# Kernel tuning notes

Measured on AMD Instinct MI355X. Metric: run time of the kernel, lower is better.

Reference implementation:

```python
import jax, jax.numpy as jnp
import numpy as np

B, S, D = 1, 2048, 2048
E, K, F = 16, 4, 512
EPS = 1e-6


def setup_inputs() -> dict:
    key = jax.random.key(0)
    ks = jax.random.split(key, 5)
    return {
        "hidden_states": jax.random.normal(ks[0], (B, S, D), dtype=jnp.float32),
        "norm_weight": jnp.ones((D,), dtype=jnp.float32),
        "gate_w": jax.random.normal(ks[1], (E, D), dtype=jnp.float32) * 0.02,
        "w_gate": jax.random.normal(ks[2], (E, D, F), dtype=jnp.float32) * 0.02,
        "w_up": jax.random.normal(ks[3], (E, D, F), dtype=jnp.float32) * 0.02,
        "w_down": jax.random.normal(ks[4], (E, F, D), dtype=jnp.float32) * 0.02,
    }


def _rmsnorm(x, w, eps=EPS):
    xf = x.astype(jnp.float32)
    var = jnp.mean(xf * xf, axis=-1, keepdims=True)
    return (xf * jax.lax.rsqrt(var + eps)).astype(x.dtype) * w


def reference(hidden_states, norm_weight, gate_w, w_gate, w_up, w_down):
    residual = hidden_states
    h = _rmsnorm(hidden_states, norm_weight)
    x = h.reshape(-1, D)                                  # [T, D], T = B*S
    T = x.shape[0]

    # Router: softmax over experts (fp32), top-k, renormalize top-k weights.
    logits = x @ gate_w.T                                  # [T, E]
    probs = jax.nn.softmax(logits.astype(jnp.float32), axis=-1)
    top_w, top_i = jax.lax.top_k(probs, K)                 # [T, K]
    top_w = top_w / jnp.sum(top_w, axis=-1, keepdims=True)
    top_w = top_w.astype(x.dtype)

    # Dense combine matrix [T, E]: routing weight if selected, else 0.
    comb = jnp.zeros((T, E), dtype=x.dtype)
    comb = comb.at[jnp.arange(T)[:, None], top_i].add(top_w)

    # Experts: SiLU-gated MLP per expert, combined with routing weights.
    g = jnp.einsum("td,edf->tef", x, w_gate)               # [T, E, F]
    u = jnp.einsum("td,edf->tef", x, w_up)                 # [T, E, F]
    act = jax.nn.silu(g) * u                               # [T, E, F]
    # Weight per-expert contributions then project down.
    y = jnp.einsum("tef,efd,te->td", act, w_down, comb)    # [T, D]

    out = residual + y.reshape(B, S, D)
    return out
```

## Files before the change

### kernel.cpp

```cpp
#include <hip/hip_runtime.h>
#include <cstdint>
#include <cstddef>

#define T_ 2048
#define D_ 2048
#define E_ 16
#define F_ 512

typedef unsigned short u16;
typedef unsigned int u32;
typedef unsigned long long u64;
typedef __attribute__((ext_vector_type(8))) short bf16x8;
typedef __attribute__((ext_vector_type(4))) float f32x4;
typedef __attribute__((ext_vector_type(2))) u32 u32x2;
typedef __attribute__((ext_vector_type(4))) u32 u32x4;
typedef __attribute__((ext_vector_type(8))) u16 u16x8;
typedef __attribute__((ext_vector_type(4))) u16 u16x4;

__device__ __forceinline__ u16 f2bf(float f){
  union { float f; u32 u; } c; c.f = f;
  return (u16)((c.u + 0x7FFFu + ((c.u >> 16) & 1u)) >> 16);
}

__device__ __forceinline__ void gload16(const void* g, void* l){
  __builtin_amdgcn_global_load_lds((const __attribute__((address_space(1))) void*)g,
                                   (__attribute__((address_space(3))) void*)l,
                                   16, 0, 0);
}

__device__ __forceinline__ u32 pk2(float a, float b){
  u32 r;
  asm("v_cvt_pk_bf16_f32 %0, %1, %2" : "=v"(r) : "v"(a), "v"(b));
  return r;
}

__global__ __launch_bounds__(256) void k_transpose_all(
    const float* __restrict__ wg, const float* __restrict__ wu, const float* __restrict__ wd,
    u16* __restrict__ wgT, u16* __restrict__ wuT, u16* __restrict__ wdT)
{
  const int bid = blockIdx.x;
  const int mat = bid >> 11;
  const int rem = bid & 2047;
  const int e = rem >> 7, within = rem & 127;
  int R, C, r0, c0;
  const float* src;
  u16* dst;
  if (mat < 2){
    R = D_; C = F_;
    r0 = (within >> 3) * 128;  c0 = (within & 7) * 64;
    src = (mat == 0) ? wg : wu;
    dst = (mat == 0) ? wgT : wuT;
  } else {
    R = F_; C = D_;
    r0 = (within & 3) * 128;  c0 = (within >> 2) * 64;
    src = wd; dst = wdT;
  }
  const int tid = threadIdx.x;
  const int br = tid >> 4;
  const int bc = tid & 15;

  const float* s = src + ((size_t)e*R + r0 + br*8)*C + c0 + bc*4;
  float col[4][8];
  #pragma unroll
  for (int j = 0; j < 8; ++j){
    const float4 t = *(const float4*)(s + (size_t)j*C);
    col[0][j] = t.x; col[1][j] = t.y; col[2][j] = t.z; col[3][j] = t.w;
  }
  u16* d = dst + ((size_t)e*C + c0 + bc*4)*R + r0 + br*8;
  #pragma unroll
  for (int c = 0; c < 4; ++c){
    u32x4 o = { pk2(col[c][0], col[c][1]), pk2(col[c][2], col[c][3]),
                pk2(col[c][4], col[c][5]), pk2(col[c][6], col[c][7]) };
    *(u32x4*)(d + (size_t)c*R) = o;
  }
}

__global__ __launch_bounds__(256) void k_norm_router(
    const float* __restrict__ x, const float* __restrict__ nw, const float* __restrict__ gw,
    u16* __restrict__ h, int* __restrict__ tok_e, float* __restrict__ tok_w)
{
  const int t = blockIdx.x, tid = threadIdx.x;
  const int lane = tid & 63, wid = tid >> 6;
  const int d0 = tid * 8;
  const float4 v0 = *(const float4*)(x + (size_t)t*D_ + d0);
  const float4 v1 = *(const float4*)(x + (size_t)t*D_ + d0 + 4);
  float hv[8] = {v0.x, v0.y, v0.z, v0.w, v1.x, v1.y, v1.z, v1.w};
  float ss = 0.f;
  #pragma unroll
  for (int j = 0; j < 8; ++j) ss += hv[j]*hv[j];
  #pragma unroll
  for (int o = 32; o; o >>= 1) ss += __shfl_xor(ss, o);
  __shared__ float sred[4];
  __shared__ float red16[4][16];
  __shared__ float lf[16];
  if (lane == 0) sred[wid] = ss;
  __syncthreads();
  const float rstd = rsqrtf((sred[0]+sred[1]+sred[2]+sred[3]) * (1.f/(float)D_) + 1e-6f);
  const float4 w0 = *(const float4*)(nw + d0);
  const float4 w1 = *(const float4*)(nw + d0 + 4);
  const float wv[8] = {w0.x,w0.y,w0.z,w0.w,w1.x,w1.y,w1.z,w1.w};
  #pragma unroll
  for (int j = 0; j < 8; ++j) hv[j] = hv[j] * rstd * wv[j];
  u16x8 hb;
  #pragma unroll
  for (int j = 0; j < 8; ++j) hb[j] = f2bf(hv[j]);
  *(u16x8*)(h + (size_t)t*D_ + d0) = hb;

  float lg[16];
  #pragma unroll
  for (int e = 0; e < 16; ++e){
    const float4 g0 = *(const float4*)(gw + e*D_ + d0);
    const float4 g1 = *(const float4*)(gw + e*D_ + d0 + 4);
    lg[e] = hv[0]*g0.x + hv[1]*g0.y + hv[2]*g0.z + hv[3]*g0.w
          + hv[4]*g1.x + hv[5]*g1.y + hv[6]*g1.z + hv[7]*g1.w;
  }
  #pragma unroll
  for (int e = 0; e < 16; ++e){
    #pragma unroll
    for (int o = 32; o; o >>= 1) lg[e] += __shfl_xor(lg[e], o);
  }
  if (lane == 0){
    #pragma unroll
    for (int e = 0; e < 16; ++e) red16[wid][e] = lg[e];
  }
  __syncthreads();
  if (tid < 16) lf[tid] = red16[0][tid] + red16[1][tid] + red16[2][tid] + red16[3][tid];
  __syncthreads();
  if (tid == 0){
    float l[16];
    #pragma unroll
    for (int e = 0; e < 16; ++e) l[e] = lf[e];
    int sel[4]; float sv[4]; u32 used = 0;
    for (int k = 0; k < 4; ++k){
      float b = -3.4e38f; int bi = 0;
      for (int e = 0; e < 16; ++e)
        if (!((used >> e) & 1u) && l[e] > b){ b = l[e]; bi = e; }
      used |= 1u << bi; sel[k] = bi; sv[k] = b;
    }
    float ex[4]; float s = 0.f;
    for (int k = 0; k < 4; ++k){ ex[k] = __expf(sv[k] - sv[0]); s += ex[k]; }
    const float inv = 1.f / s;
    int4 te = {sel[0], sel[1], sel[2], sel[3]};
    float4 tw4 = {ex[0]*inv, ex[1]*inv, ex[2]*inv, ex[3]*inv};
    *(int4*)(tok_e + t*4) = te;
    *(float4*)(tok_w + t*4) = tw4;
  }
}

__global__ __launch_bounds__(256) void k_build_lists(
    const int* __restrict__ tok_e, const float* __restrict__ tok_w,
    int* __restrict__ eidx, float* __restrict__ ew, int* __restrict__ counts)
{
  const int e = blockIdx.x, tid = threadIdx.x;
  const int lane = tid & 63, wid = tid >> 6;
  __shared__ int wtot[4];
  __shared__ int base;
  if (tid == 0) base = 0;
  __syncthreads();
  for (int t0 = 0; t0 < T_; t0 += 256){
    const int t = t0 + tid;
    const int4 te = *(const int4*)(tok_e + t*4);
    const float4 tw = *(const float4*)(tok_w + t*4);
    bool m = false; float wv = 0.f;
    if      (te.x == e){ m = true; wv = tw.x; }
    else if (te.y == e){ m = true; wv = tw.y; }
    else if (te.z == e){ m = true; wv = tw.z; }
    else if (te.w == e){ m = true; wv = tw.w; }
    const u64 mask = __ballot(m);
    const int pre = __popcll(mask & ((1ull << lane) - 1ull));
    if (lane == 0) wtot[wid] = __popcll(mask);
    __syncthreads();
    int wbase = base;
    for (int i = 0; i < wid; ++i) wbase += wtot[i];
    if (m){
      eidx[e*T_ + wbase + pre] = t;
      ew[e*T_ + wbase + pre] = wv;
    }
    __syncthreads();
    if (tid == 0) base += wtot[0] + wtot[1] + wtot[2] + wtot[3];
    __syncthreads();
  }
  if (tid == 0) counts[e] = base;
}

__global__ __launch_bounds__(256) void k_slots(
    const int* __restrict__ counts, const int* __restrict__ eidx,
    const int* __restrict__ tok_e, int* __restrict__ tok_slot)
{
  const int e = blockIdx.x;
  int abase = 0;
  for (int i = 0; i < e; ++i) abase += counts[i];
  const int cnt = counts[e];
  for (int s = threadIdx.x; s < cnt; s += 256){
    const int t = eidx[e*T_ + s];
    const int4 te = *(const int4*)(tok_e + t*4);
    const int kidx = (te.x == e) ? 0 : (te.y == e) ? 1 : (te.z == e) ? 2 : 3;
    tok_slot[t*4 + kidx] = abase + s;
  }
}

__global__ __launch_bounds__(128, 2) void k_gateup(
    const u16* __restrict__ h, const u16* __restrict__ wgT, const u16* __restrict__ wuT,
    const int* __restrict__ counts, const int* __restrict__ eidx, const float* __restrict__ ew,
    u16* __restrict__ act)
{
  const int bid = blockIdx.x;
  const int tt = bid >> 7;
  const int e  = (bid >> 3) & 15;
  const int ft = bid & 7;

  const int cnt = counts[e];
  const int row0 = tt * 128;
  if (row0 >= cnt) return;
  int abase = 0;
  for (int i = 0; i < e; ++i) abase += counts[i];

  const int tid = threadIdx.x, lane = tid & 63, w = tid >> 6;
  const int f0 = ft * 64;

  __shared__ __align__(16) u16 Xs[3][4096];
  __shared__ __align__(16) u16 Ws[3][4096];

  int* toksS = (int*)&Xs[0][0];
  if (tid < 128){
    const int slot = row0 + tid;
    const int cs = slot < cnt ? slot : (cnt - 1);
    toksS[tid] = eidx[e*T_ + cs];
  }
  __syncthreads();

  const int lr = lane >> 2, lc = lane & 3;
  const int csw = lc ^ (lr & 3) ^ ((lr >> 2) & 3);

  const u16* srcX[4]; const u16* srcW[4]; u32 dof[4];
  #pragma unroll
  for (int q = 0; q < 4; ++q){
    const int r = w*64 + q*16 + lr;
    srcX[q] = h + (size_t)toksS[r]*D_ + 8*csw;
    const u16* wb = (r < 64) ? (wgT + ((size_t)e*F_ + f0 + r)*D_)
                             : (wuT + ((size_t)e*F_ + f0 + (r - 64))*D_);
    srcW[q] = wb + 8*csw;
    dof[q] = (u32)((w*64 + q*16) * 32);
  }
  __syncthreads();

  const int p = lane & 15, g4 = lane >> 4;
  u32 aB[4], bB[8];
  #pragma unroll
  for (int m = 0; m < 4; ++m) aB[m] = (u32)((w*64 + m*16 + p) * 32);
  #pragma unroll
  for (int n = 0; n < 8; ++n) bB[n] = (u32)((n*16 + p) * 32);
  const u32 s8 = 8u * (u32)(g4 ^ (p & 3) ^ ((p >> 2) & 3));

  f32x4 acc[4][8] = {};

  #pragma unroll
  for (int b = 0; b < 2; ++b){
    const int kb = b * 32;
    #pragma unroll
    for (int q = 0; q < 4; ++q){
      gload16(srcX[q] + kb, (void*)&Xs[b][dof[q]]);
      gload16(srcW[q] + kb, (void*)&Ws[b][dof[q]]);
    }
  }

  const int NSTEP = D_ / 32;
  int cur = 0;
  for (int kt = 0; kt < NSTEP; ++kt){
    if (kt < NSTEP - 1) asm volatile("s_waitcnt vmcnt(8)" ::: "memory");
    else                asm volatile("s_waitcnt vmcnt(0)" ::: "memory");
    __builtin_amdgcn_sched_barrier(0);
    __builtin_amdgcn_s_barrier();
    __builtin_amdgcn_sched_barrier(0);
    if (kt + 2 < NSTEP){
      const int kb2 = (kt + 2) * 32;
      int nb = cur + 2; if (nb >= 3) nb -= 3;
      #pragma unroll
      for (int q = 0; q < 4; ++q){
        gload16(srcX[q] + kb2, (void*)&Xs[nb][dof[q]]);
        gload16(srcW[q] + kb2, (void*)&Ws[nb][dof[q]]);
      }
    }
    const u16* Xp = &Xs[cur][0];
    const u16* Wp = &Ws[cur][0];
    bf16x8 aF[4], bF[8];
    #pragma unroll
    for (int m = 0; m < 4; ++m) aF[m] = *(const bf16x8*)&Xp[aB[m] + s8];
    #pragma unroll
    for (int n = 0; n < 8; ++n) bF[n] = *(const bf16x8*)&Wp[bB[n] + s8];
    #pragma unroll
    for (int m = 0; m < 4; ++m)
      #pragma unroll
      for (int n = 0; n < 8; ++n)
        acc[m][n] = __builtin_amdgcn_mfma_f32_16x16x32_bf16(aF[m], bF[n], acc[m][n], 0, 0, 0);
    cur = (cur == 2) ? 0 : cur + 1;
  }

  #pragma unroll
  for (int m = 0; m < 4; ++m)
    #pragma unroll
    for (int r = 0; r < 4; ++r){
      const int row  = w*64 + m*16 + g4*4 + r;
      const int slot = row0 + row;
      if (slot < cnt){
        const float tw = ew[e*T_ + slot];
        #pragma unroll
        for (int n = 0; n < 4; ++n){
          const float gv = acc[m][n][r], uv = acc[m][n+4][r];
          const float a = tw * (gv / (1.f + __expf(-gv))) * uv;
          act[(size_t)(abase + slot)*F_ + f0 + n*16 + p] = f2bf(a);
        }
      }
    }
}

__global__ __launch_bounds__(128, 2) void k_down(
    const u16* __restrict__ act, const u16* __restrict__ wdT,
    const int* __restrict__ counts, u16* __restrict__ ydown)
{
  const int bid = blockIdx.x;
  const int tt = bid >> 8;
  const int e  = (bid >> 4) & 15;
  const int dt = bid & 15;

  const int cnt = counts[e], row0 = tt * 128;
  if (row0 >= cnt) return;
  int abase = 0;
  for (int i = 0; i < e; ++i) abase += counts[i];

  const int tid = threadIdx.x, lane = tid & 63, w = tid >> 6;
  const int d0 = dt * 128;

  __shared__ __align__(16) u16 As[3][4096];
  __shared__ __align__(16) u16 Wd[3][4096];

  const int lr = lane >> 2, lc = lane & 3;
  const int csw = lc ^ (lr & 3) ^ ((lr >> 2) & 3);

  const u16* srcX[4]; const u16* srcW[4]; u32 dof[4];
  #pragma unroll
  for (int q = 0; q < 4; ++q){
    const int r = w*64 + q*16 + lr;
    const int rs = (row0 + r < cnt) ? (row0 + r) : (cnt - 1);
    srcX[q] = act + (size_t)(abase + rs)*F_ + 8*csw;
    srcW[q] = wdT + ((size_t)e*D_ + d0 + r)*F_ + 8*csw;
    dof[q] = (u32)((w*64 + q*16) * 32);
  }

  const int p = lane & 15, g4 = lane >> 4;
  u32 aB[4], bB[8];
  #pragma unroll
  for (int m = 0; m < 4; ++m) aB[m] = (u32)((w*64 + m*16 + p) * 32);
  #pragma unroll
  for (int n = 0; n < 8; ++n) bB[n] = (u32)((n*16 + p) * 32);
  const u32 s8 = 8u * (u32)(g4 ^ (p & 3) ^ ((p >> 2) & 3));

  f32x4 acc[4][8] = {};

  #pragma unroll
  for (int b = 0; b < 2; ++b){
    const int kb = b * 32;
    #pragma unroll
    for (int q = 0; q < 4; ++q){
      gload16(srcX[q] + kb, (void*)&As[b][dof[q]]);
      gload16(srcW[q] + kb, (void*)&Wd[b][dof[q]]);
    }
  }

  const int NSTEP = F_ / 32;
  int cur = 0;
  for (int kt = 0; kt < NSTEP; ++kt){
    if (kt < NSTEP - 1) asm volatile("s_waitcnt vmcnt(8)" ::: "memory");
    else                asm volatile("s_waitcnt vmcnt(0)" ::: "memory");
    __builtin_amdgcn_sched_barrier(0);
    __builtin_amdgcn_s_barrier();
    __builtin_amdgcn_sched_barrier(0);
    if (kt + 2 < NSTEP){
      const int kb2 = (kt + 2) * 32;
      int nb = cur + 2; if (nb >= 3) nb -= 3;
      #pragma unroll
      for (int q = 0; q < 4; ++q){
        gload16(srcX[q] + kb2, (void*)&As[nb][dof[q]]);
        gload16(srcW[q] + kb2, (void*)&Wd[nb][dof[q]]);
      }
    }
    const u16* Ap = &As[cur][0];
    const u16* Wp = &Wd[cur][0];
    bf16x8 aF[4], bF[8];
    #pragma unroll
    for (int m = 0; m < 4; ++m) aF[m] = *(const bf16x8*)&Ap[aB[m] + s8];
    #pragma unroll
    for (int n = 0; n < 8; ++n) bF[n] = *(const bf16x8*)&Wp[bB[n] + s8];
    #pragma unroll
    for (int m = 0; m < 4; ++m)
      #pragma unroll
      for (int n = 0; n < 8; ++n)
        acc[m][n] = __builtin_amdgcn_mfma_f32_16x16x32_bf16(aF[m], bF[n], acc[m][n], 0, 0, 0);
    cur = (cur == 2) ? 0 : cur + 1;
  }

  #pragma unroll
  for (int m = 0; m < 4; ++m){
    #pragma unroll
    for (int r = 0; r < 4; ++r){
      const int row  = w*64 + m*16 + g4*4 + r;
      const int slot = row0 + row;
      if (slot < cnt){
        u16* yp = ydown + (size_t)(abase + slot)*D_ + d0;
        #pragma unroll
        for (int n = 0; n < 8; ++n)
          yp[n*16 + p] = f2bf(acc[m][n][r]);
      }
    }
  }
}

__global__ __launch_bounds__(256) void k_combine(
    const float* __restrict__ x, const u16* __restrict__ ydown,
    const int* __restrict__ tok_slot, float* __restrict__ out)
{
  const int t = blockIdx.x;
  const int d0 = threadIdx.x * 8;
  const int4 sl = *(const int4*)(tok_slot + t*4);
  const float4 x0 = *(const float4*)(x + (size_t)t*D_ + d0);
  const float4 x1 = *(const float4*)(x + (size_t)t*D_ + d0 + 4);
  float s[8] = {x0.x, x0.y, x0.z, x0.w, x1.x, x1.y, x1.z, x1.w};
  const int sls[4] = {sl.x, sl.y, sl.z, sl.w};
  #pragma unroll
  for (int k = 0; k < 4; ++k){
    const u16x8 v = *(const u16x8*)(ydown + (size_t)sls[k]*D_ + d0);
    #pragma unroll
    for (int j = 0; j < 8; ++j){
      union { u32 u; float f; } c; c.u = (u32)v[j] << 16;
      s[j] += c.f;
    }
  }
  float4 o0 = {s[0], s[1], s[2], s[3]};
  float4 o1 = {s[4], s[5], s[6], s[7]};
  *(float4*)(out + (size_t)t*D_ + d0)     = o0;
  *(float4*)(out + (size_t)t*D_ + d0 + 4) = o1;
}

extern "C" void kernel_launch(void* const* d_in, const int* in_sizes, int n_in,
                              void* d_out, int out_size, void* d_ws, size_t ws_size,
                              hipStream_t stream)
{
  (void)in_sizes; (void)n_in; (void)out_size; (void)ws_size;
  const float* x     = (const float*)d_in[0];
  const float* nw    = (const float*)d_in[1];
  const float* gw    = (const float*)d_in[2];
  const float* wgate = (const float*)d_in[3];
  const float* wup   = (const float*)d_in[4];
  const float* wdown = (const float*)d_in[5];
  float* out = (float*)d_out;

  char* ws = (char*)d_ws;
  u16*   h        = (u16*)(ws);
  u16*   act      = (u16*)(ws + 8388608);
  int*   counts   = (int*)(ws + 16908288);
  int*   eidx     = (int*)(ws + 16908352);
  float* ew       = (float*)(ws + 17039424);
  int*   tok_e    = (int*)(ws + 17170496);
  float* tok_w    = (float*)(ws + 17203264);
  int*   tok_slot = (int*)(ws + 17236032);
  u16*   wgT      = (u16*)(ws + 17268800);
  u16*   wuT      = (u16*)(ws + 50823232);
  u16*   wdT      = (u16*)(ws + 84377664);
  u16*   ydown    = (u16*)(ws + 17268800);

  k_transpose_all<<<6144, 256, 0, stream>>>(wgate, wup, wdown, wgT, wuT, wdT);
  k_norm_router<<<T_, 256, 0, stream>>>(x, nw, gw, h, tok_e, tok_w);
  k_build_lists<<<E_, 256, 0, stream>>>(tok_e, tok_w, eidx, ew, counts);
  k_slots<<<E_, 256, 0, stream>>>(counts, eidx, tok_e, tok_slot);
  k_gateup<<<2048, 128, 0, stream>>>(h, wgT, wuT, counts, eidx, ew, act);
  k_down<<<4096, 128, 0, stream>>>(act, wdT, counts, ydown);
  k_combine<<<T_, 256, 0, stream>>>(x, ydown, tok_slot, out);
}
```

Measured before the change: 209.2 us.

## Fuse fp32 weight transpose and bf16 conversion into the expert GEMM loaders

Removes the separate pre-pass that transposed and converted all expert weights to bf16. The gate/up and down GEMM kernels now read fp32 weights straight from global memory into registers, convert them to bf16, and write them into swizzled LDS with a double-buffered register-staged pipeline. This saves a full read-write pass over all weights. In exchange, each GEMM block re-reads fp32 weights at twice the bytes, once per token tile, and the weight prefetch is now synchronous through registers.

```diff
diff --git a/kernel.cpp b/kernel.cpp
--- a/kernel.cpp
+++ b/kernel.cpp
@@ -15,7 +15,6 @@
 typedef __attribute__((ext_vector_type(2))) u32 u32x2;
 typedef __attribute__((ext_vector_type(4))) u32 u32x4;
 typedef __attribute__((ext_vector_type(8))) u16 u16x8;
-typedef __attribute__((ext_vector_type(4))) u16 u16x4;
 
 __device__ __forceinline__ u16 f2bf(float f){
   union { float f; u32 u; } c; c.f = f;
@@ -32,47 +31,6 @@
   u32 r;
   asm("v_cvt_pk_bf16_f32 %0, %1, %2" : "=v"(r) : "v"(a), "v"(b));
   return r;
-}
-
-__global__ __launch_bounds__(256) void k_transpose_all(
-    const float* __restrict__ wg, const float* __restrict__ wu, const float* __restrict__ wd,
-    u16* __restrict__ wgT, u16* __restrict__ wuT, u16* __restrict__ wdT)
-{
-  const int bid = blockIdx.x;
-  const int mat = bid >> 11;
-  const int rem = bid & 2047;
-  const int e = rem >> 7, within = rem & 127;
-  int R, C, r0, c0;
-  const float* src;
-  u16* dst;
-  if (mat < 2){
-    R = D_; C = F_;
-    r0 = (within >> 3) * 128;  c0 = (within & 7) * 64;
-    src = (mat == 0) ? wg : wu;
-    dst = (mat == 0) ? wgT : wuT;
-  } else {
-    R = F_; C = D_;
-    r0 = (within & 3) * 128;  c0 = (within >> 2) * 64;
-    src = wd; dst = wdT;
-  }
-  const int tid = threadIdx.x;
-  const int br = tid >> 4;
-  const int bc = tid & 15;
-
-  const float* s = src + ((size_t)e*R + r0 + br*8)*C + c0 + bc*4;
-  float col[4][8];
-  #pragma unroll
-  for (int j = 0; j < 8; ++j){
-    const float4 t = *(const float4*)(s + (size_t)j*C);
-    col[0][j] = t.x; col[1][j] = t.y; col[2][j] = t.z; col[3][j] = t.w;
-  }
-  u16* d = dst + ((size_t)e*C + c0 + bc*4)*R + r0 + br*8;
-  #pragma unroll
-  for (int c = 0; c < 4; ++c){
-    u32x4 o = { pk2(col[c][0], col[c][1]), pk2(col[c][2], col[c][3]),
-                pk2(col[c][4], col[c][5]), pk2(col[c][6], col[c][7]) };
-    *(u32x4*)(d + (size_t)c*R) = o;
-  }
 }
 
 __global__ __launch_bounds__(256) void k_norm_router(
@@ -199,8 +157,27 @@
   }
 }
 
+#define WLOAD(KB, SRC, S) do {                                                 \
+    _Pragma("unroll")                                                          \
+    for (int j = 0; j < 8; ++j){                                               \
+      const float4 t_ = *(const float4*)((SRC) + (size_t)((KB) + ko*8 + j)*(S));\
+      wvf[0][j]=t_.x; wvf[1][j]=t_.y; wvf[2][j]=t_.z; wvf[3][j]=t_.w;          \
+    }                                                                          \
+  } while (0)
+
+#define WSTORE(WP) do {                                                        \
+    _Pragma("unroll")                                                          \
+    for (int i = 0; i < 4; ++i){                                               \
+      const int r_ = rg4*4 + i;                                                \
+      const u32 idx_ = (u32)(r_*32 + 8*(ko ^ (r_&3) ^ ((r_>>2)&3)));           \
+      u32x4 o_ = { pk2(wvf[i][0], wvf[i][1]), pk2(wvf[i][2], wvf[i][3]),       \
+                   pk2(wvf[i][4], wvf[i][5]), pk2(wvf[i][6], wvf[i][7]) };     \
+      *(u32x4*)&(WP)[idx_] = o_;                                               \
+    }                                                                          \
+  } while (0)
+
 __global__ __launch_bounds__(128, 2) void k_gateup(
-    const u16* __restrict__ h, const u16* __restrict__ wgT, const u16* __restrict__ wuT,
+    const u16* __restrict__ h, const float* __restrict__ wg, const float* __restrict__ wu,
     const int* __restrict__ counts, const int* __restrict__ eidx, const float* __restrict__ ew,
     u16* __restrict__ act)
 {
@@ -219,7 +196,7 @@
   const int f0 = ft * 64;
 
   __shared__ __align__(16) u16 Xs[3][4096];
-  __shared__ __align__(16) u16 Ws[3][4096];
+  __shared__ __align__(16) u16 Ws[2][4096];
 
   int* toksS = (int*)&Xs[0][0];
   if (tid < 128){
@@ -231,17 +208,16 @@
 
   const int lr = lane >> 2, lc = lane & 3;
   const int csw = lc ^ (lr & 3) ^ ((lr >> 2) & 3);
-
-  const u16* srcX[4]; const u16* srcW[4]; u32 dof[4];
+  const u16* srcX[4]; u32 dof[4];
   #pragma unroll
   for (int q = 0; q < 4; ++q){
     const int r = w*64 + q*16 + lr;
     srcX[q] = h + (size_t)toksS[r]*D_ + 8*csw;
-    const u16* wb = (r < 64) ? (wgT + ((size_t)e*F_ + f0 + r)*D_)
-                             : (wuT + ((size_t)e*F_ + f0 + (r - 64))*D_);
-    srcW[q] = wb + 8*csw;
     dof[q] = (u32)((w*64 + q*16) * 32);
   }
+  const int rg4 = tid & 31, ko = tid >> 5;
+  const float* wsel = (rg4 < 16) ? wg : wu;
+  const float* srcWf = wsel + (size_t)e*D_*F_ + f0 + ((rg4*4) & 63);
   __syncthreads();
 
   const int p = lane & 15, g4 = lane >> 4;
@@ -253,47 +229,55 @@
   const u32 s8 = 8u * (u32)(g4 ^ (p & 3) ^ ((p >> 2) & 3));
 
   f32x4 acc[4][8] = {};
-
-  #pragma unroll
-  for (int b = 0; b < 2; ++b){
-    const int kb = b * 32;
-    #pragma unroll
-    for (int q = 0; q < 4; ++q){
-      gload16(srcX[q] + kb, (void*)&Xs[b][dof[q]]);
-      gload16(srcW[q] + kb, (void*)&Ws[b][dof[q]]);
-    }
-  }
+  float wvf[4][8];
+
+  WLOAD(0, srcWf, F_);
+  #pragma unroll
+  for (int q = 0; q < 4; ++q) gload16(srcX[q],      (void*)&Xs[0][dof[q]]);
+  #pragma unroll
+  for (int q = 0; q < 4; ++q) gload16(srcX[q] + 32, (void*)&Xs[1][dof[q]]);
+  asm volatile("s_waitcnt vmcnt(8)" ::: "memory");
+  __builtin_amdgcn_sched_barrier(0);
+  WSTORE(&Ws[0][0]);
+  asm volatile("s_waitcnt vmcnt(4)" ::: "memory");
 
   const int NSTEP = D_ / 32;
-  int cur = 0;
+  int xc = 0;
   for (int kt = 0; kt < NSTEP; ++kt){
-    if (kt < NSTEP - 1) asm volatile("s_waitcnt vmcnt(8)" ::: "memory");
-    else                asm volatile("s_waitcnt vmcnt(0)" ::: "memory");
-    __builtin_amdgcn_sched_barrier(0);
+    asm volatile("s_waitcnt lgkmcnt(0)" ::: "memory");
     __builtin_amdgcn_s_barrier();
     __builtin_amdgcn_sched_barrier(0);
+    if (kt + 1 < NSTEP){
+      WLOAD((kt + 1) * 32, srcWf, F_);
+      __builtin_amdgcn_sched_barrier(0);
+    }
+    {
+      const u16* Xp = &Xs[xc][0];
+      const u16* Wp = &Ws[kt & 1][0];
+      bf16x8 aF[4], bF[8];
+      #pragma unroll
+      for (int m = 0; m < 4; ++m) aF[m] = *(const bf16x8*)&Xp[aB[m] + s8];
+      #pragma unroll
+      for (int n = 0; n < 8; ++n) bF[n] = *(const bf16x8*)&Wp[bB[n] + s8];
+      #pragma unroll
+      for (int m = 0; m < 4; ++m)
+        #pragma unroll
+        for (int n = 0; n < 8; ++n)
+          acc[m][n] = __builtin_amdgcn_mfma_f32_16x16x32_bf16(aF[m], bF[n], acc[m][n], 0, 0, 0);
+    }
     if (kt + 2 < NSTEP){
       const int kb2 = (kt + 2) * 32;
-      int nb = cur + 2; if (nb >= 3) nb -= 3;
-      #pragma unroll
-      for (int q = 0; q < 4; ++q){
-        gload16(srcX[q] + kb2, (void*)&Xs[nb][dof[q]]);
-        gload16(srcW[q] + kb2, (void*)&Ws[nb][dof[q]]);
-      }
-    }
-    const u16* Xp = &Xs[cur][0];
-    const u16* Wp = &Ws[cur][0];
-    bf16x8 aF[4], bF[8];
-    #pragma unroll
-    for (int m = 0; m < 4; ++m) aF[m] = *(const bf16x8*)&Xp[aB[m] + s8];
-    #pragma unroll
-    for (int n = 0; n < 8; ++n) bF[n] = *(const bf16x8*)&Wp[bB[n] + s8];
-    #pragma unroll
-    for (int m = 0; m < 4; ++m)
-      #pragma unroll
-      for (int n = 0; n < 8; ++n)
-        acc[m][n] = __builtin_amdgcn_mfma_f32_16x16x32_bf16(aF[m], bF[n], acc[m][n], 0, 0, 0);
-    cur = (cur == 2) ? 0 : cur + 1;
+      int nb = xc + 2; if (nb >= 3) nb -= 3;
+      #pragma unroll
+      for (int q = 0; q < 4; ++q) gload16(srcX[q] + kb2, (void*)&Xs[nb][dof[q]]);
+    }
+    if (kt + 1 < NSTEP){
+      if (kt + 2 < NSTEP) asm volatile("s_waitcnt vmcnt(4)" ::: "memory");
+      else                asm volatile("s_waitcnt vmcnt(0)" ::: "memory");
+      __builtin_amdgcn_sched_barrier(0);
+      WSTORE(&Ws[(kt + 1) & 1][0]);
+    }
+    xc = (xc == 2) ? 0 : xc + 1;
   }
 
   #pragma unroll
@@ -315,7 +299,7 @@
 }
 
 __global__ __launch_bounds__(128, 2) void k_down(
-    const u16* __restrict__ act, const u16* __restrict__ wdT,
+    const u16* __restrict__ act, const float* __restrict__ wd,
     const int* __restrict__ counts, u16* __restrict__ ydown)
 {
   const int bid = blockIdx.x;
@@ -332,20 +316,20 @@
   const int d0 = dt * 128;
 
   __shared__ __align__(16) u16 As[3][4096];
-  __shared__ __align__(16) u16 Wd[3][4096];
+  __shared__ __align__(16) u16 Wd[2][4096];
 
   const int lr = lane >> 2, lc = lane & 3;
   const int csw = lc ^ (lr & 3) ^ ((lr >> 2) & 3);
-
-  const u16* srcX[4]; const u16* srcW[4]; u32 dof[4];
+  const u16* srcX[4]; u32 dof[4];
   #pragma unroll
   for (int q = 0; q < 4; ++q){
     const int r = w*64 + q*16 + lr;
     const int rs = (row0 + r < cnt) ? (row0 + r) : (cnt - 1);
     srcX[q] = act + (size_t)(abase + rs)*F_ + 8*csw;
-    srcW[q] = wdT + ((size_t)e*D_ + d0 + r)*F_ + 8*csw;
     dof[q] = (u32)((w*64 + q*16) * 32);
   }
+  const int rg4 = tid & 31, ko = tid >> 5;
+  const float* srcWf = wd + (size_t)e*F_*D_ + d0 + rg4*4;
 
   const int p = lane & 15, g4 = lane >> 4;
   u32 aB[4], bB[8];
@@ -356,47 +340,55 @@
   const u32 s8 = 8u * (u32)(g4 ^ (p & 3) ^ ((p >> 2) & 3));
 
   f32x4 acc[4][8] = {};
-
-  #pragma unroll
-  for (int b = 0; b < 2; ++b){
-    const int kb = b * 32;
-    #pragma unroll
-    for (int q = 0; q < 4; ++q){
-      gload16(srcX[q] + kb, (void*)&As[b][dof[q]]);
-      gload16(srcW[q] + kb, (void*)&Wd[b][dof[q]]);
-    }
-  }
+  float wvf[4][8];
+
+  WLOAD(0, srcWf, D_);
+  #pragma unroll
+  for (int q = 0; q < 4; ++q) gload16(srcX[q],      (void*)&As[0][dof[q]]);
+  #pragma unroll
+  for (int q = 0; q < 4; ++q) gload16(srcX[q] + 32, (void*)&As[1][dof[q]]);
+  asm volatile("s_waitcnt vmcnt(8)" ::: "memory");
+  __builtin_amdgcn_sched_barrier(0);
+  WSTORE(&Wd[0][0]);
+  asm volatile("s_waitcnt vmcnt(4)" ::: "memory");
 
   const int NSTEP = F_ / 32;
-  int cur = 0;
+  int xc = 0;
   for (int kt = 0; kt < NSTEP; ++kt){
-    if (kt < NSTEP - 1) asm volatile("s_waitcnt vmcnt(8)" ::: "memory");
-    else                asm volatile("s_waitcnt vmcnt(0)" ::: "memory");
-    __builtin_amdgcn_sched_barrier(0);
+    asm volatile("s_waitcnt lgkmcnt(0)" ::: "memory");
     __builtin_amdgcn_s_barrier();
     __builtin_amdgcn_sched_barrier(0);
+    if (kt + 1 < NSTEP){
+      WLOAD((kt + 1) * 32, srcWf, D_);
+      __builtin_amdgcn_sched_barrier(0);
+    }
+    {
+      const u16* Ap = &As[xc][0];
+      const u16* Wp = &Wd[kt & 1][0];
+      bf16x8 aF[4], bF[8];
+      #pragma unroll
+      for (int m = 0; m < 4; ++m) aF[m] = *(const bf16x8*)&Ap[aB[m] + s8];
+      #pragma unroll
+      for (int n = 0; n < 8; ++n) bF[n] = *(const bf16x8*)&Wp[bB[n] + s8];
+      #pragma unroll
+      for (int m = 0; m < 4; ++m)
+        #pragma unroll
+        for (int n = 0; n < 8; ++n)
+          acc[m][n] = __builtin_amdgcn_mfma_f32_16x16x32_bf16(aF[m], bF[n], acc[m][n], 0, 0, 0);
+    }
     if (kt + 2 < NSTEP){
       const int kb2 = (kt + 2) * 32;
-      int nb = cur + 2; if (nb >= 3) nb -= 3;
-      #pragma unroll
-      for (int q = 0; q < 4; ++q){
-        gload16(srcX[q] + kb2, (void*)&As[nb][dof[q]]);
-        gload16(srcW[q] + kb2, (void*)&Wd[nb][dof[q]]);
-      }
-    }
-    const u16* Ap = &As[cur][0];
-    const u16* Wp = &Wd[cur][0];
-    bf16x8 aF[4], bF[8];
-    #pragma unroll
-    for (int m = 0; m < 4; ++m) aF[m] = *(const bf16x8*)&Ap[aB[m] + s8];
-    #pragma unroll
-    for (int n = 0; n < 8; ++n) bF[n] = *(const bf16x8*)&Wp[bB[n] + s8];
-    #pragma unroll
-    for (int m = 0; m < 4; ++m)
-      #pragma unroll
-      for (int n = 0; n < 8; ++n)
-        acc[m][n] = __builtin_amdgcn_mfma_f32_16x16x32_bf16(aF[m], bF[n], acc[m][n], 0, 0, 0);
-    cur = (cur == 2) ? 0 : cur + 1;
+      int nb = xc + 2; if (nb >= 3) nb -= 3;
+      #pragma unroll
+      for (int q = 0; q < 4; ++q) gload16(srcX[q] + kb2, (void*)&As[nb][dof[q]]);
+    }
+    if (kt + 1 < NSTEP){
+      if (kt + 2 < NSTEP) asm volatile("s_waitcnt vmcnt(4)" ::: "memory");
+      else                asm volatile("s_waitcnt vmcnt(0)" ::: "memory");
+      __builtin_amdgcn_sched_barrier(0);
+      WSTORE(&Wd[(kt + 1) & 1][0]);
+    }
+    xc = (xc == 2) ? 0 : xc + 1;
   }
 
   #pragma unroll
@@ -463,16 +455,12 @@
   int*   tok_e    = (int*)(ws + 17170496);
   float* tok_w    = (float*)(ws + 17203264);
   int*   tok_slot = (int*)(ws + 17236032);
-  u16*   wgT      = (u16*)(ws + 17268800);
-  u16*   wuT      = (u16*)(ws + 50823232);
-  u16*   wdT      = (u16*)(ws + 84377664);
   u16*   ydown    = (u16*)(ws + 17268800);
 
-  k_transpose_all<<<6144, 256, 0, stream>>>(wgate, wup, wdown, wgT, wuT, wdT);
   k_norm_router<<<T_, 256, 0, stream>>>(x, nw, gw, h, tok_e, tok_w);
   k_build_lists<<<E_, 256, 0, stream>>>(tok_e, tok_w, eidx, ew, counts);
   k_slots<<<E_, 256, 0, stream>>>(counts, eidx, tok_e, tok_slot);
-  k_gateup<<<2048, 128, 0, stream>>>(h, wgT, wuT, counts, eidx, ew, act);
-  k_down<<<4096, 128, 0, stream>>>(act, wdT, counts, ydown);
+  k_gateup<<<2048, 128, 0, stream>>>(h, wgate, wup, counts, eidx, ew, act);
+  k_down<<<4096, 128, 0, stream>>>(act, wdown, counts, ydown);
   k_combine<<<T_, 256, 0, stream>>>(x, ydown, tok_slot, out);
 }
```

After: 172.5 us. 17.5% less time.
